# Performance work log

Hardware: AMD Instinct MI355X
Metric: run time of the kernel (lower is better)

## Reference

```python
import jax, jax.numpy as jnp
import numpy as np

N_NODES = 50000
N_EDGES = 800000
D_IN = 128
D_OUT = 128


def setup_inputs() -> dict:
    key = jax.random.key(0)
    k1, k2, k3, k4, k5 = jax.random.split(key, 5)
    feat = jax.random.normal(k1, (N_NODES, D_IN), dtype=jnp.float32)
    W_neigh = jax.random.normal(k2, (D_OUT, D_IN), dtype=jnp.float32) * (1.0 / np.sqrt(D_IN))
    W_self = jax.random.normal(k3, (D_OUT, D_IN), dtype=jnp.float32) * (1.0 / np.sqrt(D_IN))
    b_self = jnp.zeros((D_OUT,), dtype=jnp.float32)
    src = jax.random.randint(k4, (N_EDGES,), 0, N_NODES, dtype=jnp.int32)
    dst = jax.random.randint(k5, (N_EDGES,), 0, N_NODES, dtype=jnp.int32)
    return {"feat": feat, "W_neigh": W_neigh, "W_self": W_self, "b_self": b_self, "src": src, "dst": dst}


def reference(feat, W_neigh, W_self, b_self, src, dst):
    # SAGEConv 'mean' aggregator, feat_drop=0, edge_weight=None.
    n = feat.shape[0]
    msgs = feat[src]  # copy_u gather: [E, D_IN]
    summed = jax.ops.segment_sum(msgs, dst, num_segments=n)  # [N, D_IN]
    deg = jax.ops.segment_sum(jnp.ones_like(dst, dtype=feat.dtype), dst, num_segments=n)
    h_neigh = summed / jnp.maximum(deg, 1.0)[:, None]  # fn.mean (0 for isolated nodes)
    h_neigh = h_neigh @ W_neigh.T  # fc_neigh (no bias)
    rst = feat @ W_self.T + b_self + h_neigh  # fc_self(h_self) + h_neigh
    return rst
```

## Files before the change

kernel.cpp:

```cpp
#include <hip/hip_runtime.h>
#include <hip/hip_fp8.h>
#include <cstddef>
#include <cstdint>

#define N_NODES 50000
#define N_EDGES 800000
#define D 128
#define NWG 128
#define EPW (N_EDGES / NWG)
#define NBUCK 196
#define FCONV_BLKS 3125
#define WSPLIT_BLKS 16

typedef __attribute__((ext_vector_type(8))) short bf16x8;
typedef __attribute__((ext_vector_type(16))) float f32x16;
typedef __attribute__((ext_vector_type(2))) float f32x2;

__device__ __forceinline__ unsigned short f32_to_bf16_rne(float x) {
    unsigned u = __builtin_bit_cast(unsigned, x);
    unsigned r = (u + 0x7FFFu + ((u >> 16) & 1u)) >> 16;
    return (unsigned short)r;
}
__device__ __forceinline__ float bf16lo_f32(unsigned u) {
    return __builtin_bit_cast(float, u << 16);
}
__device__ __forceinline__ float bf16hi_f32(unsigned u) {
    return __builtin_bit_cast(float, u & 0xFFFF0000u);
}

#if __has_builtin(__builtin_amdgcn_cvt_pk_fp8_f32) && __has_builtin(__builtin_amdgcn_cvt_pk_f32_fp8)
__device__ __forceinline__ unsigned fp8x4_pack(float v0, float v1, float v2, float v3) {
    int w = 0;
    w = __builtin_amdgcn_cvt_pk_fp8_f32(v0, v1, w, false);
    w = __builtin_amdgcn_cvt_pk_fp8_f32(v2, v3, w, true);
    return (unsigned)w;
}
__device__ __forceinline__ f32x2 fp8x2_lo(unsigned u) {
    return __builtin_amdgcn_cvt_pk_f32_fp8((int)u, false);
}
__device__ __forceinline__ f32x2 fp8x2_hi(unsigned u) {
    return __builtin_amdgcn_cvt_pk_f32_fp8((int)u, true);
}
#else
__device__ __forceinline__ unsigned fp8x4_pack(float v0, float v1, float v2, float v3) {
    __hip_fp8_e4m3 a(v0), b(v1), c(v2), d(v3);
    return (unsigned)a.__x | ((unsigned)b.__x << 8) | ((unsigned)c.__x << 16) | ((unsigned)d.__x << 24);
}
__device__ __forceinline__ float fp8_dec(unsigned byte) {
    __hip_fp8_e4m3 h; h.__x = (__hip_fp8_storage_t)byte;
    return (float)h;
}
__device__ __forceinline__ f32x2 fp8x2_lo(unsigned u) {
    f32x2 r; r.x = fp8_dec(u & 255u); r.y = fp8_dec((u >> 8) & 255u); return r;
}
__device__ __forceinline__ f32x2 fp8x2_hi(unsigned u) {
    f32x2 r; r.x = fp8_dec((u >> 16) & 255u); r.y = fp8_dec(u >> 24); return r;
}
#endif

__launch_bounds__(256)
__global__ void prep_kernel(const float* __restrict__ feat,
                            const float* __restrict__ Wself,
                            const float* __restrict__ Wneigh,
                            const int* __restrict__ dst,
                            unsigned short* __restrict__ featb,
                            unsigned char* __restrict__ feat8,
                            unsigned short* __restrict__ Wf,
                            int* __restrict__ ghist) {
    __shared__ int hist[256];
    const int bid = blockIdx.x;
    const int t = threadIdx.x;
    if (bid < FCONV_BLKS) {
        const int i = bid * 256 + t;
        if (i >= N_NODES * D / 8) return;
        const float* gp = feat + (size_t)i * 8;
        const float4 a = *(const float4*)gp;
        const float4 b = *(const float4*)(gp + 4);
        bf16x8 h;
        h[0] = (short)f32_to_bf16_rne(a.x); h[1] = (short)f32_to_bf16_rne(a.y);
        h[2] = (short)f32_to_bf16_rne(a.z); h[3] = (short)f32_to_bf16_rne(a.w);
        h[4] = (short)f32_to_bf16_rne(b.x); h[5] = (short)f32_to_bf16_rne(b.y);
        h[6] = (short)f32_to_bf16_rne(b.z); h[7] = (short)f32_to_bf16_rne(b.w);
        *(bf16x8*)&featb[(size_t)i * 8] = h;
        uint2 q;
        q.x = fp8x4_pack(a.x, a.y, a.z, a.w);
        q.y = fp8x4_pack(b.x, b.y, b.z, b.w);
        *(uint2*)&feat8[(size_t)i * 8] = q;
    } else if (bid < FCONV_BLKS + WSPLIT_BLKS) {
        const int unit = (bid - FCONV_BLKS) * 256 + t;
        if (unit >= 4096) return;
        const int phase = unit >> 11;
        const int kbi   = (unit >> 9) & 3;
        const int u     = unit & 511;
        const int j     = u & 127;
        const int c     = u >> 7;
        const float* __restrict__ W = phase ? Wneigh : Wself;
        const float* gp = &W[(size_t)j * D + kbi * 32 + c * 8];
        const int p = j >> 5, ks = c >> 1, g = c & 1;
        const size_t base = (size_t)(phase * 4 + kbi) * 4096
                          + (size_t)(((p * 2 + ks) * 64) + (j & 31) + 32 * g) * 8;
#pragma unroll
        for (int e = 0; e < 8; ++e)
            Wf[base + e] = f32_to_bf16_rne(gp[e]);
    } else {
        const int w = bid - FCONV_BLKS - WSPLIT_BLKS;
        hist[t] = 0;
        __syncthreads();
        const int base = w * EPW;
        for (int i = t; i < EPW; i += 256)
            atomicAdd(&hist[dst[base + i] >> 8], 1);
        __syncthreads();
        ghist[w * 256 + t] = hist[t];
    }
}

__launch_bounds__(256)
__global__ void s3_bin_kernel(const int* __restrict__ src,
                              const int* __restrict__ dst,
                              const int* __restrict__ ghist,
                              unsigned* __restrict__ binned,
                              int* __restrict__ gboff) {
    __shared__ int s[256];
    __shared__ int cur[256];
    const int t = threadIdx.x;
    const int w = blockIdx.x;
    int tot = 0, mypre = 0;
    for (int w2 = 0; w2 < NWG; ++w2) {
        const int v = ghist[w2 * 256 + t];
        tot += v;
        if (w2 < w) mypre += v;
    }
    s[t] = tot;
    __syncthreads();
    for (int d = 1; d < 256; d <<= 1) {
        int v = 0;
        if (t >= d) v = s[t - d];
        __syncthreads();
        s[t] += v;
        __syncthreads();
    }
    const int boff = s[t] - tot;
    if (w == 0) {
        gboff[t] = boff;
        if (t == 255) gboff[256] = s[255];
    }
    cur[t] = boff + mypre;
    __syncthreads();
    const int base = w * EPW;
    for (int i = t; i < EPW; i += 256) {
        const int sv = src[base + i];
        const int d = dst[base + i];
        const int p = atomicAdd(&cur[d >> 8], 1);
        binned[p] = (unsigned)sv | ((unsigned)(d & 255) << 16);
    }
}

__launch_bounds__(256)
__global__ void finalize_kernel(const unsigned* __restrict__ binned,
                                const int* __restrict__ gboff,
                                int* __restrict__ deg_i,
                                int* __restrict__ off,
                                unsigned short* __restrict__ csr_src) {
    __shared__ int c0[256];
    __shared__ int s[256];
    __shared__ int cur[256];
    const int t = threadIdx.x;
    const int b = blockIdx.x;
    c0[t] = 0;
    __syncthreads();
    const int lo = gboff[b], hi = gboff[b + 1];
    for (int i = lo + t; i < hi; i += 256)
        atomicAdd(&c0[(binned[i] >> 16) & 255u], 1);
    __syncthreads();
    const int c = c0[t];
    s[t] = c;
    __syncthreads();
    for (int d = 1; d < 256; d <<= 1) {
        int v = 0;
        if (t >= d) v = s[t - d];
        __syncthreads();
        s[t] += v;
        __syncthreads();
    }
    const int o = gboff[b] + s[t] - c;
    const int node = b * 256 + t;
    if (node < N_NODES) {
        deg_i[node] = c;
        off[node] = o;
    }
    cur[t] = o;
    __syncthreads();
    for (int i = lo + t; i < hi; i += 256) {
        const unsigned u = binned[i];
        const int p = atomicAdd(&cur[(u >> 16) & 255u], 1);
        csr_src[p] = (unsigned short)(u & 0xFFFFu);
    }
}

__launch_bounds__(256)
__global__ void gather_kernel(const unsigned char* __restrict__ feat8,
                              const int* __restrict__ off,
                              const int* __restrict__ deg_i,
                              const unsigned short* __restrict__ csr_src,
                              unsigned short* __restrict__ hneighb) {
    const int t = threadIdx.x;
    const int lane8 = (t & 15) * 8;
    const int node = blockIdx.x * 16 + (t >> 4);
    if (node >= N_NODES) return;
    const int s0 = off[node];
    const int cnt = deg_i[node];
    const int end = s0 + cnt;
    float a0 = 0.f, a1 = 0.f, a2 = 0.f, a3 = 0.f;
    float a4 = 0.f, a5 = 0.f, a6 = 0.f, a7 = 0.f;
    int e = s0;
#define ACC(u) { const f32x2 p0 = fp8x2_lo((u).x); const f32x2 p1 = fp8x2_hi((u).x); \
                 const f32x2 p2 = fp8x2_lo((u).y); const f32x2 p3 = fp8x2_hi((u).y); \
                 a0 += p0.x; a1 += p0.y; a2 += p1.x; a3 += p1.y; \
                 a4 += p2.x; a5 += p2.y; a6 += p3.x; a7 += p3.y; }
    for (; e + 8 <= end; e += 8) {
        const int i0 = csr_src[e];
        const int i1 = csr_src[e + 1];
        const int i2 = csr_src[e + 2];
        const int i3 = csr_src[e + 3];
        const int i4 = csr_src[e + 4];
        const int i5 = csr_src[e + 5];
        const int i6 = csr_src[e + 6];
        const int i7 = csr_src[e + 7];
        const uint2 u0 = *(const uint2*)&feat8[(size_t)i0 * D + lane8];
        const uint2 u1 = *(const uint2*)&feat8[(size_t)i1 * D + lane8];
        const uint2 u2 = *(const uint2*)&feat8[(size_t)i2 * D + lane8];
        const uint2 u3 = *(const uint2*)&feat8[(size_t)i3 * D + lane8];
        const uint2 u4 = *(const uint2*)&feat8[(size_t)i4 * D + lane8];
        const uint2 u5 = *(const uint2*)&feat8[(size_t)i5 * D + lane8];
        const uint2 u6 = *(const uint2*)&feat8[(size_t)i6 * D + lane8];
        const uint2 u7 = *(const uint2*)&feat8[(size_t)i7 * D + lane8];
        ACC(u0); ACC(u1); ACC(u2); ACC(u3);
        ACC(u4); ACC(u5); ACC(u6); ACC(u7);
    }
    for (; e + 4 <= end; e += 4) {
        const int i0 = csr_src[e];
        const int i1 = csr_src[e + 1];
        const int i2 = csr_src[e + 2];
        const int i3 = csr_src[e + 3];
        const uint2 u0 = *(const uint2*)&feat8[(size_t)i0 * D + lane8];
        const uint2 u1 = *(const uint2*)&feat8[(size_t)i1 * D + lane8];
        const uint2 u2 = *(const uint2*)&feat8[(size_t)i2 * D + lane8];
        const uint2 u3 = *(const uint2*)&feat8[(size_t)i3 * D + lane8];
        ACC(u0); ACC(u1); ACC(u2); ACC(u3);
    }
    for (; e < end; ++e) {
        const uint2 u = *(const uint2*)&feat8[(size_t)csr_src[e] * D + lane8];
        ACC(u);
    }
#undef ACC
    const float sc = 1.f / fmaxf((float)cnt, 1.f);
    const unsigned h0 = f32_to_bf16_rne(a0 * sc);
    const unsigned h1 = f32_to_bf16_rne(a1 * sc);
    const unsigned h2 = f32_to_bf16_rne(a2 * sc);
    const unsigned h3 = f32_to_bf16_rne(a3 * sc);
    const unsigned h4 = f32_to_bf16_rne(a4 * sc);
    const unsigned h5 = f32_to_bf16_rne(a5 * sc);
    const unsigned h6 = f32_to_bf16_rne(a6 * sc);
    const unsigned h7 = f32_to_bf16_rne(a7 * sc);
    uint4 o;
    o.x = (h1 << 16) | h0;
    o.y = (h3 << 16) | h2;
    o.z = (h5 << 16) | h4;
    o.w = (h7 << 16) | h6;
    *(uint4*)&hneighb[(size_t)node * D + lane8] = o;
}

__launch_bounds__(256)
__global__ void gemm_kernel(const unsigned short* __restrict__ featb,
                            const unsigned short* __restrict__ hneighb,
                            const unsigned short* __restrict__ Wf,
                            const float* __restrict__ bias,
                            float* __restrict__ out) {
    __shared__ __align__(16) unsigned short sW[32768];
    __shared__ __align__(16) unsigned short sA[2][4096];

    const int tid  = threadIdx.x;
    const int wv   = tid >> 6;
    const int l    = tid & 63;
    const int row0 = blockIdx.x * 128;

#pragma unroll
    for (int i = 0; i < 16; ++i) {
        const int o = (i * 256 + tid) * 8;
        *(bf16x8*)&sW[o] = *(const bf16x8*)&Wf[o];
    }

    auto stageA = [&](int sel, int blk) {
        const int kbi = blk & 3;
        const unsigned short* __restrict__ A = (blk < 4) ? featb : hneighb;
#pragma unroll
        for (int i = 0; i < 2; ++i) {
            const int u   = i * 256 + tid;
            const int row = u & 127;
            const int c   = u >> 7;
            const int grow = row0 + row;
            bf16x8 v = {};
            if (grow < N_NODES)
                v = *(const bf16x8*)&A[(size_t)grow * D + kbi * 32 + c * 8];
            const int p = row >> 5, ks = c >> 1, g = c & 1;
            const int o = ((p * 2 + ks) * 64 + (row & 31) + 32 * g) * 8;
            *(bf16x8*)&sA[sel][o] = v;
        }
    };

    f32x16 acc[4] = {};

    stageA(0, 0);
    __syncthreads();
#pragma unroll 1
    for (int blk = 0; blk < 8; ++blk) {
        const int cur = blk & 1;
        if (blk < 7) stageA(cur ^ 1, blk + 1);
        const int wbase = blk * 4096;
#pragma unroll
        for (int ks = 0; ks < 2; ++ks) {
            const bf16x8 a = *(const bf16x8*)&sA[cur][((wv * 2 + ks) * 64 + l) * 8];
#pragma unroll
            for (int n = 0; n < 4; ++n) {
                const bf16x8 w = *(const bf16x8*)&sW[wbase + ((n * 2 + ks) * 64 + l) * 8];
                acc[n] = __builtin_amdgcn_mfma_f32_32x32x16_bf16(a, w, acc[n], 0, 0, 0);
            }
        }
        __syncthreads();
    }

    const int col = l & 31;
    const int hi2 = l >> 5;
    float bv[4];
#pragma unroll
    for (int n = 0; n < 4; ++n) bv[n] = bias[n * 32 + col];
#pragma unroll
    for (int r = 0; r < 16; ++r) {
        const int rloc = (r & 3) + 8 * (r >> 2) + 4 * hi2;
        const int grow = row0 + wv * 32 + rloc;
        if (grow < N_NODES) {
#pragma unroll
            for (int n = 0; n < 4; ++n)
                out[(size_t)grow * D + n * 32 + col] = acc[n][r] + bv[n];
        }
    }
}

extern "C" void kernel_launch(void* const* d_in, const int* in_sizes, int n_in,
                              void* d_out, int out_size, void* d_ws, size_t ws_size,
                              hipStream_t stream) {
    const float* feat  = (const float*)d_in[0];
    const float* Wn    = (const float*)d_in[1];
    const float* Wsf   = (const float*)d_in[2];
    const float* bself = (const float*)d_in[3];
    const int*   src   = (const int*)d_in[4];
    const int*   dst   = (const int*)d_in[5];
    float* out = (float*)d_out;

    unsigned short* featb   = (unsigned short*)d_ws;
    unsigned short* hneighb = featb + (size_t)N_NODES * D;
    unsigned* binned = (unsigned*)(hneighb + (size_t)N_NODES * D);
    unsigned short* csr_src = (unsigned short*)(binned + N_EDGES);
    int*   deg_i     = (int*)(csr_src + N_EDGES);
    int*   off       = deg_i + N_NODES;
    int*   ghist     = off + N_NODES;
    int*   gboff     = ghist + NWG * 256;
    unsigned short* Wf = (unsigned short*)(gboff + 320);
    unsigned char* feat8 = (unsigned char*)(Wf + 8 * 4096);

    prep_kernel<<<FCONV_BLKS + WSPLIT_BLKS + NWG, 256, 0, stream>>>(
        feat, Wsf, Wn, dst, featb, feat8, Wf, ghist);
    s3_bin_kernel<<<NWG, 256, 0, stream>>>(src, dst, ghist, binned, gboff);
    finalize_kernel<<<NBUCK, 256, 0, stream>>>(binned, gboff, deg_i, off, csr_src);
    gather_kernel<<<(N_NODES + 15) / 16, 256, 0, stream>>>(feat8, off, deg_i, csr_src, hneighb);

    const int gblocks = (N_NODES + 127) / 128;
    gemm_kernel<<<gblocks, 256, 0, stream>>>(featb, hneighb, Wf, bself, out);
}
```

Baseline: 80.83 us.

## Gather neighbor features per-thread-per-node over feature slices with sliced output layout

Changes the gather kernel from 16 threads per node with 8-byte fp8 loads to one thread per node handling a 16-byte feature slice, with 8 slices spread across blocks. The aggregated output is stored in a slice-major layout, and the GEMM's A staging is changed to read that layout. The aim is fewer threads doing index/offset loads and wider per-load transactions. The cost is that each thread walks its node's full edge list serially and loads are less coalesced across a wavefront, with load imbalance between nodes of different degree.

```diff
diff --git a/kernel.cpp b/kernel.cpp
--- a/kernel.cpp
+++ b/kernel.cpp
@@ -11,6 +11,7 @@
 #define NBUCK 196
 #define FCONV_BLKS 3125
 #define WSPLIT_BLKS 16
+#define SLICE_STRIDE (N_NODES * 16)
 
 typedef __attribute__((ext_vector_type(8))) short bf16x8;
 typedef __attribute__((ext_vector_type(16))) float f32x16;
@@ -20,12 +21,6 @@
     unsigned u = __builtin_bit_cast(unsigned, x);
     unsigned r = (u + 0x7FFFu + ((u >> 16) & 1u)) >> 16;
     return (unsigned short)r;
-}
-__device__ __forceinline__ float bf16lo_f32(unsigned u) {
-    return __builtin_bit_cast(float, u << 16);
-}
-__device__ __forceinline__ float bf16hi_f32(unsigned u) {
-    return __builtin_bit_cast(float, u & 0xFFFF0000u);
 }
 
 #if __has_builtin(__builtin_amdgcn_cvt_pk_fp8_f32) && __has_builtin(__builtin_amdgcn_cvt_pk_f32_fp8)
@@ -204,70 +199,55 @@
                               const unsigned short* __restrict__ csr_src,
                               unsigned short* __restrict__ hneighb) {
     const int t = threadIdx.x;
-    const int lane8 = (t & 15) * 8;
-    const int node = blockIdx.x * 16 + (t >> 4);
+    const int slice = blockIdx.x & 7;
+    const int nb    = blockIdx.x >> 3;
+    const int node  = nb * 256 + t;
     if (node >= N_NODES) return;
     const int s0 = off[node];
     const int cnt = deg_i[node];
     const int end = s0 + cnt;
-    float a0 = 0.f, a1 = 0.f, a2 = 0.f, a3 = 0.f;
-    float a4 = 0.f, a5 = 0.f, a6 = 0.f, a7 = 0.f;
-    int e = s0;
+    const size_t fofs = (size_t)slice * 16;
+
+    float a[16];
+#pragma unroll
+    for (int k = 0; k < 16; ++k) a[k] = 0.f;
+
 #define ACC(u) { const f32x2 p0 = fp8x2_lo((u).x); const f32x2 p1 = fp8x2_hi((u).x); \
                  const f32x2 p2 = fp8x2_lo((u).y); const f32x2 p3 = fp8x2_hi((u).y); \
-                 a0 += p0.x; a1 += p0.y; a2 += p1.x; a3 += p1.y; \
-                 a4 += p2.x; a5 += p2.y; a6 += p3.x; a7 += p3.y; }
-    for (; e + 8 <= end; e += 8) {
-        const int i0 = csr_src[e];
-        const int i1 = csr_src[e + 1];
-        const int i2 = csr_src[e + 2];
-        const int i3 = csr_src[e + 3];
-        const int i4 = csr_src[e + 4];
-        const int i5 = csr_src[e + 5];
-        const int i6 = csr_src[e + 6];
-        const int i7 = csr_src[e + 7];
-        const uint2 u0 = *(const uint2*)&feat8[(size_t)i0 * D + lane8];
-        const uint2 u1 = *(const uint2*)&feat8[(size_t)i1 * D + lane8];
-        const uint2 u2 = *(const uint2*)&feat8[(size_t)i2 * D + lane8];
-        const uint2 u3 = *(const uint2*)&feat8[(size_t)i3 * D + lane8];
-        const uint2 u4 = *(const uint2*)&feat8[(size_t)i4 * D + lane8];
-        const uint2 u5 = *(const uint2*)&feat8[(size_t)i5 * D + lane8];
-        const uint2 u6 = *(const uint2*)&feat8[(size_t)i6 * D + lane8];
-        const uint2 u7 = *(const uint2*)&feat8[(size_t)i7 * D + lane8];
-        ACC(u0); ACC(u1); ACC(u2); ACC(u3);
-        ACC(u4); ACC(u5); ACC(u6); ACC(u7);
-    }
+                 const f32x2 p4 = fp8x2_lo((u).z); const f32x2 p5 = fp8x2_hi((u).z); \
+                 const f32x2 p6 = fp8x2_lo((u).w); const f32x2 p7 = fp8x2_hi((u).w); \
+                 a[0] += p0.x; a[1] += p0.y; a[2]  += p1.x; a[3]  += p1.y; \
+                 a[4] += p2.x; a[5] += p2.y; a[6]  += p3.x; a[7]  += p3.y; \
+                 a[8] += p4.x; a[9] += p4.y; a[10] += p5.x; a[11] += p5.y; \
+                 a[12] += p6.x; a[13] += p6.y; a[14] += p7.x; a[15] += p7.y; }
+
+    int e = s0;
     for (; e + 4 <= end; e += 4) {
         const int i0 = csr_src[e];
         const int i1 = csr_src[e + 1];
         const int i2 = csr_src[e + 2];
         const int i3 = csr_src[e + 3];
-        const uint2 u0 = *(const uint2*)&feat8[(size_t)i0 * D + lane8];
-        const uint2 u1 = *(const uint2*)&feat8[(size_t)i1 * D + lane8];
-        const uint2 u2 = *(const uint2*)&feat8[(size_t)i2 * D + lane8];
-        const uint2 u3 = *(const uint2*)&feat8[(size_t)i3 * D + lane8];
+        const uint4 u0 = *(const uint4*)&feat8[(size_t)i0 * D + fofs];
+        const uint4 u1 = *(const uint4*)&feat8[(size_t)i1 * D + fofs];
+        const uint4 u2 = *(const uint4*)&feat8[(size_t)i2 * D + fofs];
+        const uint4 u3 = *(const uint4*)&feat8[(size_t)i3 * D + fofs];
         ACC(u0); ACC(u1); ACC(u2); ACC(u3);
     }
     for (; e < end; ++e) {
-        const uint2 u = *(const uint2*)&feat8[(size_t)csr_src[e] * D + lane8];
+        const uint4 u = *(const uint4*)&feat8[(size_t)csr_src[e] * D + fofs];
         ACC(u);
     }
 #undef ACC
+
     const float sc = 1.f / fmaxf((float)cnt, 1.f);
-    const unsigned h0 = f32_to_bf16_rne(a0 * sc);
-    const unsigned h1 = f32_to_bf16_rne(a1 * sc);
-    const unsigned h2 = f32_to_bf16_rne(a2 * sc);
-    const unsigned h3 = f32_to_bf16_rne(a3 * sc);
-    const unsigned h4 = f32_to_bf16_rne(a4 * sc);
-    const unsigned h5 = f32_to_bf16_rne(a5 * sc);
-    const unsigned h6 = f32_to_bf16_rne(a6 * sc);
-    const unsigned h7 = f32_to_bf16_rne(a7 * sc);
-    uint4 o;
-    o.x = (h1 << 16) | h0;
-    o.y = (h3 << 16) | h2;
-    o.z = (h5 << 16) | h4;
-    o.w = (h7 << 16) | h6;
-    *(uint4*)&hneighb[(size_t)node * D + lane8] = o;
+    unsigned short* op = &hneighb[(size_t)slice * SLICE_STRIDE + (size_t)node * 16];
+    bf16x8 o0, o1;
+#pragma unroll
+    for (int k = 0; k < 8; ++k) o0[k] = (short)f32_to_bf16_rne(a[k] * sc);
+#pragma unroll
+    for (int k = 0; k < 8; ++k) o1[k] = (short)f32_to_bf16_rne(a[8 + k] * sc);
+    *(bf16x8*)op = o0;
+    *(bf16x8*)(op + 8) = o1;
 }
 
 __launch_bounds__(256)
@@ -292,7 +272,6 @@
 
     auto stageA = [&](int sel, int blk) {
         const int kbi = blk & 3;
-        const unsigned short* __restrict__ A = (blk < 4) ? featb : hneighb;
 #pragma unroll
         for (int i = 0; i < 2; ++i) {
             const int u   = i * 256 + tid;
@@ -300,8 +279,15 @@
             const int c   = u >> 7;
             const int grow = row0 + row;
             bf16x8 v = {};
-            if (grow < N_NODES)
-                v = *(const bf16x8*)&A[(size_t)grow * D + kbi * 32 + c * 8];
+            if (grow < N_NODES) {
+                if (blk < 4) {
+                    v = *(const bf16x8*)&featb[(size_t)grow * D + kbi * 32 + c * 8];
+                } else {
+                    const int slice = 2 * kbi + (c >> 1);
+                    v = *(const bf16x8*)&hneighb[(size_t)slice * SLICE_STRIDE
+                                                 + (size_t)grow * 16 + (c & 1) * 8];
+                }
+            }
             const int p = row >> 5, ks = c >> 1, g = c & 1;
             const int o = ((p * 2 + ks) * 64 + (row & 31) + 32 * g) * 8;
             *(bf16x8*)&sA[sel][o] = v;
@@ -372,7 +358,7 @@
         feat, Wsf, Wn, dst, featb, feat8, Wf, ghist);
     s3_bin_kernel<<<NWG, 256, 0, stream>>>(src, dst, ghist, binned, gboff);
     finalize_kernel<<<NBUCK, 256, 0, stream>>>(binned, gboff, deg_i, off, csr_src);
-    gather_kernel<<<(N_NODES + 15) / 16, 256, 0, stream>>>(feat8, off, deg_i, csr_src, hneighb);
+    gather_kernel<<<NBUCK * 8, 256, 0, stream>>>(feat8, off, deg_i, csr_src, hneighb);
 
     const int gblocks = (N_NODES + 127) / 128;
     gemm_kernel<<<gblocks, 256, 0, stream>>>(featb, hneighb, Wf, bself, out);
```

Measured after the change: 133.3 us. 64.9% more time.

## Split neighbor gather into two feature-half slices with sliced hneigh layout

Applied to the files above, without the earlier changes.

The gather kernel now splits each node's 128 features into two 64-wide halves handled by alternating blocks, with 8 threads per node-half instead of 16 threads per full row. hneigh is stored as two planar slices of 64 columns, and the GEMM's A-staging indexes into the matching slice. The aim is more parallelism and fewer edges per wave in flight, which may improve latency hiding on the random gathers. In exchange, every CSR index and offset is read twice, and each row gather becomes a 64-byte access per half.

```diff
diff --git a/kernel.cpp b/kernel.cpp
--- a/kernel.cpp
+++ b/kernel.cpp
@@ -11,6 +11,7 @@
 #define NBUCK 196
 #define FCONV_BLKS 3125
 #define WSPLIT_BLKS 16
+#define SLICE2 (N_NODES * 64)
 
 typedef __attribute__((ext_vector_type(8))) short bf16x8;
 typedef __attribute__((ext_vector_type(16))) float f32x16;
@@ -20,12 +21,6 @@
     unsigned u = __builtin_bit_cast(unsigned, x);
     unsigned r = (u + 0x7FFFu + ((u >> 16) & 1u)) >> 16;
     return (unsigned short)r;
-}
-__device__ __forceinline__ float bf16lo_f32(unsigned u) {
-    return __builtin_bit_cast(float, u << 16);
-}
-__device__ __forceinline__ float bf16hi_f32(unsigned u) {
-    return __builtin_bit_cast(float, u & 0xFFFF0000u);
 }
 
 #if __has_builtin(__builtin_amdgcn_cvt_pk_fp8_f32) && __has_builtin(__builtin_amdgcn_cvt_pk_f32_fp8)
@@ -204,12 +199,15 @@
                               const unsigned short* __restrict__ csr_src,
                               unsigned short* __restrict__ hneighb) {
     const int t = threadIdx.x;
-    const int lane8 = (t & 15) * 8;
-    const int node = blockIdx.x * 16 + (t >> 4);
+    const int slice = blockIdx.x & 1;
+    const int node  = (blockIdx.x >> 1) * 32 + (t >> 3);
+    const int l3    = t & 7;
     if (node >= N_NODES) return;
     const int s0 = off[node];
     const int cnt = deg_i[node];
     const int end = s0 + cnt;
+    const size_t fofs = (size_t)slice * 64 + l3 * 8;
+
     float a0 = 0.f, a1 = 0.f, a2 = 0.f, a3 = 0.f;
     float a4 = 0.f, a5 = 0.f, a6 = 0.f, a7 = 0.f;
     int e = s0;
@@ -226,14 +224,14 @@
         const int i5 = csr_src[e + 5];
         const int i6 = csr_src[e + 6];
         const int i7 = csr_src[e + 7];
-        const uint2 u0 = *(const uint2*)&feat8[(size_t)i0 * D + lane8];
-        const uint2 u1 = *(const uint2*)&feat8[(size_t)i1 * D + lane8];
-        const uint2 u2 = *(const uint2*)&feat8[(size_t)i2 * D + lane8];
-        const uint2 u3 = *(const uint2*)&feat8[(size_t)i3 * D + lane8];
-        const uint2 u4 = *(const uint2*)&feat8[(size_t)i4 * D + lane8];
-        const uint2 u5 = *(const uint2*)&feat8[(size_t)i5 * D + lane8];
-        const uint2 u6 = *(const uint2*)&feat8[(size_t)i6 * D + lane8];
-        const uint2 u7 = *(const uint2*)&feat8[(size_t)i7 * D + lane8];
+        const uint2 u0 = *(const uint2*)&feat8[(size_t)i0 * D + fofs];
+        const uint2 u1 = *(const uint2*)&feat8[(size_t)i1 * D + fofs];
+        const uint2 u2 = *(const uint2*)&feat8[(size_t)i2 * D + fofs];
+        const uint2 u3 = *(const uint2*)&feat8[(size_t)i3 * D + fofs];
+        const uint2 u4 = *(const uint2*)&feat8[(size_t)i4 * D + fofs];
+        const uint2 u5 = *(const uint2*)&feat8[(size_t)i5 * D + fofs];
+        const uint2 u6 = *(const uint2*)&feat8[(size_t)i6 * D + fofs];
+        const uint2 u7 = *(const uint2*)&feat8[(size_t)i7 * D + fofs];
         ACC(u0); ACC(u1); ACC(u2); ACC(u3);
         ACC(u4); ACC(u5); ACC(u6); ACC(u7);
     }
@@ -242,32 +240,28 @@
         const int i1 = csr_src[e + 1];
         const int i2 = csr_src[e + 2];
         const int i3 = csr_src[e + 3];
-        const uint2 u0 = *(const uint2*)&feat8[(size_t)i0 * D + lane8];
-        const uint2 u1 = *(const uint2*)&feat8[(size_t)i1 * D + lane8];
-        const uint2 u2 = *(const uint2*)&feat8[(size_t)i2 * D + lane8];
-        const uint2 u3 = *(const uint2*)&feat8[(size_t)i3 * D + lane8];
+        const uint2 u0 = *(const uint2*)&feat8[(size_t)i0 * D + fofs];
+        const uint2 u1 = *(const uint2*)&feat8[(size_t)i1 * D + fofs];
+        const uint2 u2 = *(const uint2*)&feat8[(size_t)i2 * D + fofs];
+        const uint2 u3 = *(const uint2*)&feat8[(size_t)i3 * D + fofs];
         ACC(u0); ACC(u1); ACC(u2); ACC(u3);
     }
     for (; e < end; ++e) {
-        const uint2 u = *(const uint2*)&feat8[(size_t)csr_src[e] * D + lane8];
+        const uint2 u = *(const uint2*)&feat8[(size_t)csr_src[e] * D + fofs];
         ACC(u);
     }
 #undef ACC
     const float sc = 1.f / fmaxf((float)cnt, 1.f);
-    const unsigned h0 = f32_to_bf16_rne(a0 * sc);
-    const unsigned h1 = f32_to_bf16_rne(a1 * sc);
-    const unsigned h2 = f32_to_bf16_rne(a2 * sc);
-    const unsigned h3 = f32_to_bf16_rne(a3 * sc);
-    const unsigned h4 = f32_to_bf16_rne(a4 * sc);
-    const unsigned h5 = f32_to_bf16_rne(a5 * sc);
-    const unsigned h6 = f32_to_bf16_rne(a6 * sc);
-    const unsigned h7 = f32_to_bf16_rne(a7 * sc);
-    uint4 o;
-    o.x = (h1 << 16) | h0;
-    o.y = (h3 << 16) | h2;
-    o.z = (h5 << 16) | h4;
-    o.w = (h7 << 16) | h6;
-    *(uint4*)&hneighb[(size_t)node * D + lane8] = o;
+    bf16x8 o;
+    o[0] = (short)f32_to_bf16_rne(a0 * sc);
+    o[1] = (short)f32_to_bf16_rne(a1 * sc);
+    o[2] = (short)f32_to_bf16_rne(a2 * sc);
+    o[3] = (short)f32_to_bf16_rne(a3 * sc);
+    o[4] = (short)f32_to_bf16_rne(a4 * sc);
+    o[5] = (short)f32_to_bf16_rne(a5 * sc);
+    o[6] = (short)f32_to_bf16_rne(a6 * sc);
+    o[7] = (short)f32_to_bf16_rne(a7 * sc);
+    *(bf16x8*)&hneighb[(size_t)slice * SLICE2 + (size_t)node * 64 + l3 * 8] = o;
 }
 
 __launch_bounds__(256)
@@ -292,7 +286,6 @@
 
     auto stageA = [&](int sel, int blk) {
         const int kbi = blk & 3;
-        const unsigned short* __restrict__ A = (blk < 4) ? featb : hneighb;
 #pragma unroll
         for (int i = 0; i < 2; ++i) {
             const int u   = i * 256 + tid;
@@ -300,8 +293,14 @@
             const int c   = u >> 7;
             const int grow = row0 + row;
             bf16x8 v = {};
-            if (grow < N_NODES)
-                v = *(const bf16x8*)&A[(size_t)grow * D + kbi * 32 + c * 8];
+            if (grow < N_NODES) {
+                if (blk < 4) {
+                    v = *(const bf16x8*)&featb[(size_t)grow * D + kbi * 32 + c * 8];
+                } else {
+                    v = *(const bf16x8*)&hneighb[(size_t)(kbi >> 1) * SLICE2
+                                                 + (size_t)grow * 64 + (kbi & 1) * 32 + c * 8];
+                }
+            }
             const int p = row >> 5, ks = c >> 1, g = c & 1;
             const int o = ((p * 2 + ks) * 64 + (row & 31) + 32 * g) * 8;
             *(bf16x8*)&sA[sel][o] = v;
@@ -372,7 +371,9 @@
         feat, Wsf, Wn, dst, featb, feat8, Wf, ghist);
     s3_bin_kernel<<<NWG, 256, 0, stream>>>(src, dst, ghist, binned, gboff);
     finalize_kernel<<<NBUCK, 256, 0, stream>>>(binned, gboff, deg_i, off, csr_src);
-    gather_kernel<<<(N_NODES + 15) / 16, 256, 0, stream>>>(feat8, off, deg_i, csr_src, hneighb);
+
+    const int gb = 2 * ((N_NODES + 31) / 32);
+    gather_kernel<<<gb, 256, 0, stream>>>(feat8, off, deg_i, csr_src, hneighb);
 
     const int gblocks = (N_NODES + 127) / 128;
     gemm_kernel<<<gblocks, 256, 0, stream>>>(featb, hneighb, Wf, bself, out);
```

After: 84.64 us. 4.7% more time.
